# Kernel tuning notes

Measured on AMD Instinct MI355X. Metric: run time of the kernel, lower is better.

The kernel has to match this reference:

```python
import jax, jax.numpy as jnp
import numpy as np

DELTA_V = 0.5
DELTA_D = 1.5
KSEG = 17  # segment ids 0..16 (0 = background)
EPS = 1e-12


def setup_inputs() -> dict:
    key = jax.random.key(0)
    k1, k2, k3 = jax.random.split(key, 3)
    B, C, H, W = 8, 8, 512, 512
    embeddings = jax.random.normal(k1, (B, C, H, W), dtype=jnp.float32)
    instance_labels = jax.random.randint(k2, (B, H, W), 0, KSEG, dtype=jnp.int32)
    mask = jax.random.randint(k3, (B, H, W), 0, 2, dtype=jnp.int32)
    return {"embeddings": embeddings, "instance_labels": instance_labels, "mask": mask}


def _discriminative_loss(embeddings, inst):
    # embeddings: (B, C, H, W); inst: (B, H, W) int, 0 = ignore/background
    B, C, H, W = embeddings.shape
    N = H * W
    ids = inst.reshape(B, N)
    # global segment ids so one segment_sum handles all batches
    gids = (ids + jnp.arange(B, dtype=ids.dtype)[:, None] * KSEG).reshape(-1)  # (B*N,)
    e = embeddings.reshape(B, C, N).transpose(0, 2, 1).reshape(B * N, C)       # (B*N, C)

    counts = jax.ops.segment_sum(jnp.ones((B * N,), embeddings.dtype), gids, num_segments=B * KSEG)
    sums = jax.ops.segment_sum(e, gids, num_segments=B * KSEG)                 # (B*KSEG, C)
    means = sums / jnp.maximum(counts, 1.0)[:, None]

    # ---- pull: per-pixel hinged distance to its instance mean ----
    diff = e - means[gids]                                                      # (B*N, C)
    d = jnp.sqrt(jnp.maximum(jnp.sum(diff * diff, axis=-1), EPS))               # (B*N,)
    pen = jnp.maximum(d - DELTA_V, 0.0) ** 2
    pen_mean = jax.ops.segment_sum(pen, gids, num_segments=B * KSEG) / jnp.maximum(counts, 1.0)

    counts_bk = counts.reshape(B, KSEG)
    pen_mean_bk = pen_mean.reshape(B, KSEG)
    present = (counts_bk > 0) & (jnp.arange(KSEG)[None, :] != 0)                # (B, KSEG) bool
    presentf = present.astype(embeddings.dtype)
    K = presentf.sum(axis=-1)                                                   # (B,) instances per image
    pull_b = (pen_mean_bk * presentf).sum(axis=-1) / jnp.maximum(K, 1.0)

    # ---- push: hinged pairwise mean distances ----
    mu = means.reshape(B, KSEG, C)
    dm = mu[:, :, None, :] - mu[:, None, :, :]                                  # (B, K, K, C)
    dist = jnp.sqrt(jnp.maximum(jnp.sum(dm * dm, axis=-1), EPS))
    hinge = jnp.maximum(2.0 * DELTA_D - dist, 0.0) ** 2
    iu = jnp.triu(jnp.ones((KSEG, KSEG), bool), k=1)                            # i < j
    pair_mask = (present[:, :, None] & present[:, None, :] & iu[None]).astype(embeddings.dtype)
    n_pairs = pair_mask.sum(axis=(-1, -2))
    push_b = (hinge * pair_mask).sum(axis=(-1, -2)) / jnp.maximum(n_pairs, 1.0)

    validf = (K > 0).astype(embeddings.dtype)
    nvalid = jnp.maximum(validf.sum(), 1.0)
    loss_pull = (pull_b * validf).sum() / nvalid
    loss_push = (push_b * validf).sum() / nvalid
    return loss_pull, loss_push


def reference(embeddings, instance_labels, mask):
    inst = instance_labels * mask  # zero out non-TCL pixels
    return _discriminative_loss(embeddings, inst)
```

## Files before the change

kernel.cpp:

```cpp
#include <hip/hip_runtime.h>

#define BATCH 8
#define CCH 8
#define HW 262144
#define SEGS 16
#define GX 256


__global__ __launch_bounds__(256, 4) void accum_kernel(
    const float* __restrict__ emb, const int* __restrict__ lab,
    const int* __restrict__ msk, float* __restrict__ ws)
{
    const int b = blockIdx.y;
    const int wave = threadIdx.x >> 6;
    __shared__ float lsum[4][SEGS][CCH];
    __shared__ float lcnt[4][SEGS];
    for (int i = threadIdx.x; i < 4 * SEGS * CCH; i += 256) (&lsum[0][0][0])[i] = 0.f;
    for (int i = threadIdx.x; i < 4 * SEGS; i += 256) (&lcnt[0][0])[i] = 0.f;
    __syncthreads();

    const int g = blockIdx.x * 256 + threadIdx.x;

    const int4 l4 = ((const int4*)(lab + (size_t)b * HW))[g];
    const int4 m4 = ((const int4*)(msk + (size_t)b * HW))[g];
    const float4* ep = (const float4*)(emb + (size_t)b * CCH * HW);
    float4 e[CCH];
#pragma unroll
    for (int c = 0; c < CCH; ++c) e[c] = ep[(size_t)c * (HW / 4) + g];

    const int id0 = m4.x ? l4.x : 0;
    const int id1 = m4.y ? l4.y : 0;
    const int id2 = m4.z ? l4.z : 0;
    const int id3 = m4.w ? l4.w : 0;

    if (id0) atomicAdd(&lcnt[wave][id0 - 1], 1.f);
    if (id1) atomicAdd(&lcnt[wave][id1 - 1], 1.f);
    if (id2) atomicAdd(&lcnt[wave][id2 - 1], 1.f);
    if (id3) atomicAdd(&lcnt[wave][id3 - 1], 1.f);
#pragma unroll
    for (int c = 0; c < CCH; ++c) {
        if (id0) atomicAdd(&lsum[wave][id0 - 1][c], e[c].x);
        if (id1) atomicAdd(&lsum[wave][id1 - 1][c], e[c].y);
        if (id2) atomicAdd(&lsum[wave][id2 - 1][c], e[c].z);
        if (id3) atomicAdd(&lsum[wave][id3 - 1][c], e[c].w);
    }

    __syncthreads();
    for (int i = threadIdx.x; i < SEGS * CCH; i += 256) {
        float v = (&lsum[0][0][0])[i] + (&lsum[1][0][0])[i]
                + (&lsum[2][0][0])[i] + (&lsum[3][0][0])[i];
        if (v != 0.f) atomicAdd(&ws[128 + b * SEGS * CCH + i], v);
    }
    for (int i = threadIdx.x; i < SEGS; i += 256) {
        float v = lcnt[0][i] + lcnt[1][i] + lcnt[2][i] + lcnt[3][i];
        if (v != 0.f) atomicAdd(&ws[b * SEGS + i], v);
    }
}

__global__ __launch_bounds__(256, 4) void pull_kernel(
    const float* __restrict__ emb, const int* __restrict__ lab,
    const int* __restrict__ msk, float* __restrict__ ws)
{
    const int b = blockIdx.y;
    const int wave = threadIdx.x >> 6;
    __shared__ float mt[CCH][SEGS];
    __shared__ float lpen[4][SEGS];
    for (int i = threadIdx.x; i < 4 * SEGS; i += 256) (&lpen[0][0])[i] = 0.f;
    if (threadIdx.x < SEGS * CCH) {
        int s = threadIdx.x & (SEGS - 1);
        int c = threadIdx.x >> 4;
        float cv = ws[b * SEGS + s];
        mt[c][s] = ws[128 + (b * SEGS + s) * CCH + c] / fmaxf(cv, 1.0f);
    }
    __syncthreads();

    const int g = blockIdx.x * 256 + threadIdx.x;

    const int4 l4 = ((const int4*)(lab + (size_t)b * HW))[g];
    const int4 m4 = ((const int4*)(msk + (size_t)b * HW))[g];
    const float4* ep = (const float4*)(emb + (size_t)b * CCH * HW);
    float4 e[CCH];
#pragma unroll
    for (int c = 0; c < CCH; ++c) e[c] = ep[(size_t)c * (HW / 4) + g];

    const int id0 = m4.x ? l4.x : 0;
    const int id1 = m4.y ? l4.y : 0;
    const int id2 = m4.z ? l4.z : 0;
    const int id3 = m4.w ? l4.w : 0;
    const int ix0 = id0 ? id0 - 1 : 0;
    const int ix1 = id1 ? id1 - 1 : 0;
    const int ix2 = id2 ? id2 - 1 : 0;
    const int ix3 = id3 ? id3 - 1 : 0;

    float ss0 = 0.f, ss1 = 0.f, ss2 = 0.f, ss3 = 0.f;
#pragma unroll
    for (int c = 0; c < CCH; ++c) {
        float d0 = e[c].x - mt[c][ix0];
        float d1 = e[c].y - mt[c][ix1];
        float d2 = e[c].z - mt[c][ix2];
        float d3 = e[c].w - mt[c][ix3];
        ss0 = fmaf(d0, d0, ss0);
        ss1 = fmaf(d1, d1, ss1);
        ss2 = fmaf(d2, d2, ss2);
        ss3 = fmaf(d3, d3, ss3);
    }
    if (id0) { float d = sqrtf(fmaxf(ss0, 1e-12f)); float h = fmaxf(d - 0.5f, 0.f); atomicAdd(&lpen[wave][ix0], h * h); }
    if (id1) { float d = sqrtf(fmaxf(ss1, 1e-12f)); float h = fmaxf(d - 0.5f, 0.f); atomicAdd(&lpen[wave][ix1], h * h); }
    if (id2) { float d = sqrtf(fmaxf(ss2, 1e-12f)); float h = fmaxf(d - 0.5f, 0.f); atomicAdd(&lpen[wave][ix2], h * h); }
    if (id3) { float d = sqrtf(fmaxf(ss3, 1e-12f)); float h = fmaxf(d - 0.5f, 0.f); atomicAdd(&lpen[wave][ix3], h * h); }

    __syncthreads();
    for (int i = threadIdx.x; i < SEGS; i += 256) {
        float v = lpen[0][i] + lpen[1][i] + lpen[2][i] + lpen[3][i];
        if (v != 0.f) atomicAdd(&ws[1152 + b * SEGS + i], v);
    }
}

__global__ __launch_bounds__(256) void finalize_kernel(
    const float* __restrict__ ws, float* __restrict__ out)
{
    __shared__ float cnt[BATCH][SEGS];
    __shared__ float mu[BATCH][SEGS][CCH];
    __shared__ float pen[BATCH][SEGS];
    __shared__ float res[BATCH][3];

    for (int i = threadIdx.x; i < BATCH * SEGS; i += 256) {
        (&cnt[0][0])[i] = ws[i];
        (&pen[0][0])[i] = ws[1152 + i];
    }
    for (int i = threadIdx.x; i < BATCH * SEGS * CCH; i += 256) {
        float c = ws[i / CCH];
        (&mu[0][0][0])[i] = ws[128 + i] / fmaxf(c, 1.0f);
    }
    __syncthreads();

    const int b = threadIdx.x >> 5;
    const int l = threadIdx.x & 31;

    float pullv = 0.f, Kf = 0.f;
    if (l < SEGS && cnt[b][l] > 0.f) {
        Kf = 1.f;
        pullv = pen[b][l] / cnt[b][l];
    }
    float hs = 0.f, np = 0.f;
    for (int p = l; p < 256; p += 32) {
        int i = p >> 4, j = p & 15;
        if (i < j && cnt[b][i] > 0.f && cnt[b][j] > 0.f) {
            float ssq = 0.f;
#pragma unroll
            for (int c = 0; c < CCH; ++c) {
                float d = mu[b][i][c] - mu[b][j][c];
                ssq += d * d;
            }
            float dist = sqrtf(fmaxf(ssq, 1e-12f));
            float h = fmaxf(3.0f - dist, 0.f);
            hs += h * h;
            np += 1.f;
        }
    }
#pragma unroll
    for (int m = 16; m >= 1; m >>= 1) {
        pullv += __shfl_xor(pullv, m);
        Kf    += __shfl_xor(Kf, m);
        hs    += __shfl_xor(hs, m);
        np    += __shfl_xor(np, m);
    }
    if (l == 0) {
        res[b][0] = (Kf > 0.f) ? pullv / Kf : 0.f;
        res[b][1] = (np > 0.f) ? hs / np : 0.f;
        res[b][2] = (Kf > 0.f) ? 1.f : 0.f;
    }
    __syncthreads();
    if (threadIdx.x == 0) {
        float sp = 0.f, sh = 0.f, nv = 0.f;
        for (int bb = 0; bb < BATCH; ++bb) {
            sp += res[bb][0] * res[bb][2];
            sh += res[bb][1] * res[bb][2];
            nv += res[bb][2];
        }
        nv = fmaxf(nv, 1.f);
        out[0] = sp / nv;
        out[1] = sh / nv;
    }
}

extern "C" void kernel_launch(void* const* d_in, const int* in_sizes, int n_in,
                              void* d_out, int out_size, void* d_ws, size_t ws_size,
                              hipStream_t stream)
{
    const float* emb = (const float*)d_in[0];
    const int* lab = (const int*)d_in[1];
    const int* msk = (const int*)d_in[2];
    float* out = (float*)d_out;
    float* ws = (float*)d_ws;

    hipMemsetAsync(d_ws, 0, 1280 * sizeof(float), stream);
    dim3 grid(GX, BATCH);
    accum_kernel<<<grid, 256, 0, stream>>>(emb, lab, msk, ws);
    pull_kernel<<<grid, 256, 0, stream>>>(emb, lab, msk, ws);
    finalize_kernel<<<1, 256, 0, stream>>>(ws, out);
}
```

Measured before the change: 162.3 us.

## Replace global atomics with per-block partials and drop workspace memset

Each block now handles four chunks of pixels in a loop (grid 64x8 instead of 256x8) and writes its per-segment count, sum and penalty partials to a distinct workspace slot instead of using global atomicAdd. The pull kernel and the finalize kernel reduce those partials deterministically, which removes the hipMemsetAsync launch and the global atomic contention. In exchange the grid has fewer blocks, which may hide memory latency less well on a large GPU, and every pull block redundantly re-reduces the 64 partials for its batch.

After: 159.9 us. About the same (-1.5%).

```diff
diff --git a/kernel.cpp b/kernel.cpp
--- a/kernel.cpp
+++ b/kernel.cpp
@@ -4,116 +4,137 @@
 #define CCH 8
 #define HW 262144
 #define SEGS 16
-#define GX 256
-
-
-__global__ __launch_bounds__(256, 4) void accum_kernel(
+#define XB 64
+#define GPB (HW / 4 / XB)
+#define NITER (GPB / 256)
+
+#define P1 0
+#define MEANS 73728
+#define PP 74880
+
+__global__ __launch_bounds__(256) void accum_kernel(
     const float* __restrict__ emb, const int* __restrict__ lab,
     const int* __restrict__ msk, float* __restrict__ ws)
 {
-    const int b = blockIdx.y;
-    const int wave = threadIdx.x >> 6;
+    const int b = blockIdx.y, xb = blockIdx.x;
+    const int tid = threadIdx.x, wave = tid >> 6;
     __shared__ float lsum[4][SEGS][CCH];
     __shared__ float lcnt[4][SEGS];
-    for (int i = threadIdx.x; i < 4 * SEGS * CCH; i += 256) (&lsum[0][0][0])[i] = 0.f;
-    for (int i = threadIdx.x; i < 4 * SEGS; i += 256) (&lcnt[0][0])[i] = 0.f;
-    __syncthreads();
-
-    const int g = blockIdx.x * 256 + threadIdx.x;
-
-    const int4 l4 = ((const int4*)(lab + (size_t)b * HW))[g];
-    const int4 m4 = ((const int4*)(msk + (size_t)b * HW))[g];
+    for (int i = tid; i < 4 * SEGS * CCH; i += 256) (&lsum[0][0][0])[i] = 0.f;
+    for (int i = tid; i < 4 * SEGS; i += 256) (&lcnt[0][0])[i] = 0.f;
+    __syncthreads();
+
+    const int4* lb = (const int4*)(lab + (size_t)b * HW);
+    const int4* mb = (const int4*)(msk + (size_t)b * HW);
     const float4* ep = (const float4*)(emb + (size_t)b * CCH * HW);
-    float4 e[CCH];
-#pragma unroll
-    for (int c = 0; c < CCH; ++c) e[c] = ep[(size_t)c * (HW / 4) + g];
-
-    const int id0 = m4.x ? l4.x : 0;
-    const int id1 = m4.y ? l4.y : 0;
-    const int id2 = m4.z ? l4.z : 0;
-    const int id3 = m4.w ? l4.w : 0;
-
-    if (id0) atomicAdd(&lcnt[wave][id0 - 1], 1.f);
-    if (id1) atomicAdd(&lcnt[wave][id1 - 1], 1.f);
-    if (id2) atomicAdd(&lcnt[wave][id2 - 1], 1.f);
-    if (id3) atomicAdd(&lcnt[wave][id3 - 1], 1.f);
-#pragma unroll
-    for (int c = 0; c < CCH; ++c) {
-        if (id0) atomicAdd(&lsum[wave][id0 - 1][c], e[c].x);
-        if (id1) atomicAdd(&lsum[wave][id1 - 1][c], e[c].y);
-        if (id2) atomicAdd(&lsum[wave][id2 - 1][c], e[c].z);
-        if (id3) atomicAdd(&lsum[wave][id3 - 1][c], e[c].w);
-    }
-
-    __syncthreads();
-    for (int i = threadIdx.x; i < SEGS * CCH; i += 256) {
-        float v = (&lsum[0][0][0])[i] + (&lsum[1][0][0])[i]
-                + (&lsum[2][0][0])[i] + (&lsum[3][0][0])[i];
-        if (v != 0.f) atomicAdd(&ws[128 + b * SEGS * CCH + i], v);
-    }
-    for (int i = threadIdx.x; i < SEGS; i += 256) {
-        float v = lcnt[0][i] + lcnt[1][i] + lcnt[2][i] + lcnt[3][i];
-        if (v != 0.f) atomicAdd(&ws[b * SEGS + i], v);
-    }
-}
-
-__global__ __launch_bounds__(256, 4) void pull_kernel(
+    const int base = xb * GPB;
+
+#pragma unroll
+    for (int q = 0; q < NITER; ++q) {
+        const int g = base + q * 256 + tid;
+        int4 l4 = lb[g];
+        int4 m4 = mb[g];
+        float4 e[CCH];
+#pragma unroll
+        for (int c = 0; c < CCH; ++c) e[c] = ep[(size_t)c * (HW / 4) + g];
+
+        const int id0 = m4.x ? l4.x : 0;
+        const int id1 = m4.y ? l4.y : 0;
+        const int id2 = m4.z ? l4.z : 0;
+        const int id3 = m4.w ? l4.w : 0;
+        if (id0) atomicAdd(&lcnt[wave][id0 - 1], 1.f);
+        if (id1) atomicAdd(&lcnt[wave][id1 - 1], 1.f);
+        if (id2) atomicAdd(&lcnt[wave][id2 - 1], 1.f);
+        if (id3) atomicAdd(&lcnt[wave][id3 - 1], 1.f);
+#pragma unroll
+        for (int c = 0; c < CCH; ++c) {
+            if (id0) atomicAdd(&lsum[wave][id0 - 1][c], e[c].x);
+            if (id1) atomicAdd(&lsum[wave][id1 - 1][c], e[c].y);
+            if (id2) atomicAdd(&lsum[wave][id2 - 1][c], e[c].z);
+            if (id3) atomicAdd(&lsum[wave][id3 - 1][c], e[c].w);
+        }
+    }
+    __syncthreads();
+
+    float* dst = ws + P1 + (b * XB + xb) * 144;
+    if (tid < SEGS)
+        dst[tid] = lcnt[0][tid] + lcnt[1][tid] + lcnt[2][tid] + lcnt[3][tid];
+    if (tid < SEGS * CCH)
+        dst[16 + tid] = (&lsum[0][0][0])[tid] + (&lsum[1][0][0])[tid]
+                      + (&lsum[2][0][0])[tid] + (&lsum[3][0][0])[tid];
+}
+
+__global__ __launch_bounds__(256) void pull_kernel(
     const float* __restrict__ emb, const int* __restrict__ lab,
     const int* __restrict__ msk, float* __restrict__ ws)
 {
-    const int b = blockIdx.y;
-    const int wave = threadIdx.x >> 6;
+    const int b = blockIdx.y, xb = blockIdx.x;
+    const int tid = threadIdx.x, wave = tid >> 6;
+    __shared__ float sred[144];
     __shared__ float mt[CCH][SEGS];
     __shared__ float lpen[4][SEGS];
-    for (int i = threadIdx.x; i < 4 * SEGS; i += 256) (&lpen[0][0])[i] = 0.f;
-    if (threadIdx.x < SEGS * CCH) {
-        int s = threadIdx.x & (SEGS - 1);
-        int c = threadIdx.x >> 4;
-        float cv = ws[b * SEGS + s];
-        mt[c][s] = ws[128 + (b * SEGS + s) * CCH + c] / fmaxf(cv, 1.0f);
-    }
-    __syncthreads();
-
-    const int g = blockIdx.x * 256 + threadIdx.x;
-
-    const int4 l4 = ((const int4*)(lab + (size_t)b * HW))[g];
-    const int4 m4 = ((const int4*)(msk + (size_t)b * HW))[g];
+
+    if (tid < 144) {
+        const float* p = ws + P1 + (size_t)b * XB * 144 + tid;
+        float acc = 0.f;
+#pragma unroll 8
+        for (int k = 0; k < XB; ++k) acc += p[k * 144];
+        sred[tid] = acc;
+        if (xb == 0) ws[MEANS + b * 144 + tid] = acc;
+    }
+    if (tid >= 144 && tid < 144 + 64) (&lpen[0][0])[tid - 144] = 0.f;
+    __syncthreads();
+    if (tid < SEGS * CCH) {
+        int s = tid & (SEGS - 1);
+        int c = tid >> 4;
+        mt[c][s] = sred[16 + s * CCH + c] / fmaxf(sred[s], 1.0f);
+    }
+    __syncthreads();
+
+    const int4* lb = (const int4*)(lab + (size_t)b * HW);
+    const int4* mb = (const int4*)(msk + (size_t)b * HW);
     const float4* ep = (const float4*)(emb + (size_t)b * CCH * HW);
-    float4 e[CCH];
-#pragma unroll
-    for (int c = 0; c < CCH; ++c) e[c] = ep[(size_t)c * (HW / 4) + g];
-
-    const int id0 = m4.x ? l4.x : 0;
-    const int id1 = m4.y ? l4.y : 0;
-    const int id2 = m4.z ? l4.z : 0;
-    const int id3 = m4.w ? l4.w : 0;
-    const int ix0 = id0 ? id0 - 1 : 0;
-    const int ix1 = id1 ? id1 - 1 : 0;
-    const int ix2 = id2 ? id2 - 1 : 0;
-    const int ix3 = id3 ? id3 - 1 : 0;
-
-    float ss0 = 0.f, ss1 = 0.f, ss2 = 0.f, ss3 = 0.f;
-#pragma unroll
-    for (int c = 0; c < CCH; ++c) {
-        float d0 = e[c].x - mt[c][ix0];
-        float d1 = e[c].y - mt[c][ix1];
-        float d2 = e[c].z - mt[c][ix2];
-        float d3 = e[c].w - mt[c][ix3];
-        ss0 = fmaf(d0, d0, ss0);
-        ss1 = fmaf(d1, d1, ss1);
-        ss2 = fmaf(d2, d2, ss2);
-        ss3 = fmaf(d3, d3, ss3);
-    }
-    if (id0) { float d = sqrtf(fmaxf(ss0, 1e-12f)); float h = fmaxf(d - 0.5f, 0.f); atomicAdd(&lpen[wave][ix0], h * h); }
-    if (id1) { float d = sqrtf(fmaxf(ss1, 1e-12f)); float h = fmaxf(d - 0.5f, 0.f); atomicAdd(&lpen[wave][ix1], h * h); }
-    if (id2) { float d = sqrtf(fmaxf(ss2, 1e-12f)); float h = fmaxf(d - 0.5f, 0.f); atomicAdd(&lpen[wave][ix2], h * h); }
-    if (id3) { float d = sqrtf(fmaxf(ss3, 1e-12f)); float h = fmaxf(d - 0.5f, 0.f); atomicAdd(&lpen[wave][ix3], h * h); }
-
-    __syncthreads();
-    for (int i = threadIdx.x; i < SEGS; i += 256) {
-        float v = lpen[0][i] + lpen[1][i] + lpen[2][i] + lpen[3][i];
-        if (v != 0.f) atomicAdd(&ws[1152 + b * SEGS + i], v);
-    }
+    const int base = xb * GPB;
+
+#pragma unroll
+    for (int q = 0; q < NITER; ++q) {
+        const int g = base + q * 256 + tid;
+        int4 l4 = lb[g];
+        int4 m4 = mb[g];
+        float4 e[CCH];
+#pragma unroll
+        for (int c = 0; c < CCH; ++c) e[c] = ep[(size_t)c * (HW / 4) + g];
+
+        const int id0 = m4.x ? l4.x : 0;
+        const int id1 = m4.y ? l4.y : 0;
+        const int id2 = m4.z ? l4.z : 0;
+        const int id3 = m4.w ? l4.w : 0;
+        const int ix0 = id0 ? id0 - 1 : 0;
+        const int ix1 = id1 ? id1 - 1 : 0;
+        const int ix2 = id2 ? id2 - 1 : 0;
+        const int ix3 = id3 ? id3 - 1 : 0;
+
+        float ss0 = 0.f, ss1 = 0.f, ss2 = 0.f, ss3 = 0.f;
+#pragma unroll
+        for (int c = 0; c < CCH; ++c) {
+            float d0 = e[c].x - mt[c][ix0];
+            float d1 = e[c].y - mt[c][ix1];
+            float d2 = e[c].z - mt[c][ix2];
+            float d3 = e[c].w - mt[c][ix3];
+            ss0 = fmaf(d0, d0, ss0);
+            ss1 = fmaf(d1, d1, ss1);
+            ss2 = fmaf(d2, d2, ss2);
+            ss3 = fmaf(d3, d3, ss3);
+        }
+        if (id0) { float d = sqrtf(fmaxf(ss0, 1e-12f)); float h = fmaxf(d - 0.5f, 0.f); atomicAdd(&lpen[wave][ix0], h * h); }
+        if (id1) { float d = sqrtf(fmaxf(ss1, 1e-12f)); float h = fmaxf(d - 0.5f, 0.f); atomicAdd(&lpen[wave][ix1], h * h); }
+        if (id2) { float d = sqrtf(fmaxf(ss2, 1e-12f)); float h = fmaxf(d - 0.5f, 0.f); atomicAdd(&lpen[wave][ix2], h * h); }
+        if (id3) { float d = sqrtf(fmaxf(ss3, 1e-12f)); float h = fmaxf(d - 0.5f, 0.f); atomicAdd(&lpen[wave][ix3], h * h); }
+    }
+    __syncthreads();
+    if (tid < SEGS)
+        ws[PP + (b * XB + xb) * 16 + tid] =
+            lpen[0][tid] + lpen[1][tid] + lpen[2][tid] + lpen[3][tid];
 }
 
 __global__ __launch_bounds__(256) void finalize_kernel(
@@ -124,13 +145,27 @@
     __shared__ float pen[BATCH][SEGS];
     __shared__ float res[BATCH][3];
 
-    for (int i = threadIdx.x; i < BATCH * SEGS; i += 256) {
-        (&cnt[0][0])[i] = ws[i];
-        (&pen[0][0])[i] = ws[1152 + i];
-    }
+    for (int i = threadIdx.x; i < BATCH * 144; i += 256) {
+        int bb = i / 144, t = i - bb * 144;
+        float v = ws[MEANS + i];
+        if (t < SEGS) cnt[bb][t] = v;
+        else {
+            int idx = t - 16;
+            mu[bb][idx >> 3][idx & 7] = v;
+        }
+    }
+    if (threadIdx.x < BATCH * SEGS) {
+        int bb = threadIdx.x >> 4, s = threadIdx.x & 15;
+        const float* p = ws + PP + (size_t)bb * XB * 16 + s;
+        float acc = 0.f;
+#pragma unroll 8
+        for (int k = 0; k < XB; ++k) acc += p[k * 16];
+        pen[bb][s] = acc;
+    }
+    __syncthreads();
     for (int i = threadIdx.x; i < BATCH * SEGS * CCH; i += 256) {
-        float c = ws[i / CCH];
-        (&mu[0][0][0])[i] = ws[128 + i] / fmaxf(c, 1.0f);
+        int bb = i >> 7, r = i & 127;
+        mu[bb][r >> 3][r & 7] /= fmaxf(cnt[bb][r >> 3], 1.0f);
     }
     __syncthreads();
 
@@ -194,8 +229,7 @@
     float* out = (float*)d_out;
     float* ws = (float*)d_ws;
 
-    hipMemsetAsync(d_ws, 0, 1280 * sizeof(float), stream);
-    dim3 grid(GX, BATCH);
+    dim3 grid(XB, BATCH);
     accum_kernel<<<grid, 256, 0, stream>>>(emb, lab, msk, ws);
     pull_kernel<<<grid, 256, 0, stream>>>(emb, lab, msk, ws);
     finalize_kernel<<<1, 256, 0, stream>>>(ws, out);
```
